# Kernel tuning notes

Measured on AMD Instinct MI355X. Metric: run time of the kernel, lower is better.

## Reference

```python
import jax, jax.numpy as jnp
import numpy as np

B, C, H, W = 1, 12, 256, 256
T = 8          # time_steps
F = 64         # recurrent/conv filters
SIGMA = 1.0


def _to_c(x):
    return jax.lax.complex(x[..., 0], x[..., 1])


def _to_r(x):
    return jnp.stack([jnp.real(x), jnp.imag(x)], axis=-1)


def _fft2c(x):  # orthogonal centered 2D FFT over last two dims (complex input)
    x = jnp.fft.ifftshift(x, axes=(-2, -1))
    x = jnp.fft.fft2(x, axes=(-2, -1), norm='ortho')
    return jnp.fft.fftshift(x, axes=(-2, -1))


def _ifft2c(x):
    x = jnp.fft.ifftshift(x, axes=(-2, -1))
    x = jnp.fft.ifft2(x, axes=(-2, -1), norm='ortho')
    return jnp.fft.fftshift(x, axes=(-2, -1))


def _conv(x, w, b=None, dilation=1):
    k = w.shape[-1]
    pad = dilation * (k - 1) // 2  # 'same' padding as ConvNonlinear
    y = jax.lax.conv_general_dilated(x, w, (1, 1), [(pad, pad), (pad, pad)],
                                     rhs_dilation=(dilation, dilation),
                                     dimension_numbers=('NCHW', 'OIHW', 'NCHW'))
    if b is not None:
        y = y + b[None, :, None, None]
    return y


def _gru(x, h, ih_w, ih_b, hh_w, hh_b):  # ConvGRUCell
    i_r, i_z, i_n = jnp.split(_conv(x, ih_w, ih_b), 3, axis=1)
    h_r, h_z, h_n = jnp.split(_conv(h, hh_w, hh_b), 3, axis=1)
    r = jax.nn.sigmoid(i_r + h_r)
    z = jax.nn.sigmoid(i_z + h_z)
    n = jnp.tanh(i_n + r * h_n)
    return (1.0 - z) * n + z * h


def setup_inputs():
    key = jax.random.key(0)
    ks = jax.random.split(key, 16)
    rn = lambda k, s, sc=1.0: jax.random.normal(k, s, jnp.float32) * sc
    return {
        'pred': rn(ks[0], (B, C, H, W, 2)),
        'masked_kspace': rn(ks[1], (B, C, H, W, 2)),
        'sense': rn(ks[2], (B, C, H, W, 2), 0.1),
        'mask': jax.random.randint(ks[3], (B, 1, H, W, 1), 0, 2).astype(bool),
        'conv1_w': rn(ks[4], (F, 4, 5, 5), 0.05),
        'conv1_b': jnp.zeros((F,), jnp.float32),
        'gru1_ih_w': rn(ks[5], (3 * F, F, 1, 1), 0.05),
        'gru1_ih_b': jnp.zeros((3 * F,), jnp.float32),
        'gru1_hh_w': rn(ks[6], (3 * F, F, 1, 1), 0.05),
        'gru1_hh_b': jnp.zeros((3 * F,), jnp.float32),
        'conv2_w': rn(ks[7], (F, F, 3, 3), 0.05),
        'conv2_b': jnp.zeros((F,), jnp.float32),
        'gru2_ih_w': rn(ks[8], (3 * F, F, 1, 1), 0.05),
        'gru2_ih_b': jnp.zeros((3 * F,), jnp.float32),
        'gru2_hh_w': rn(ks[9], (3 * F, F, 1, 1), 0.05),
        'gru2_hh_b': jnp.zeros((3 * F,), jnp.float32),
        'final_w': rn(ks[10], (2, F, 3, 3), 0.05),
        'dc_weight': jnp.ones((1,), jnp.float32),
    }


def reference(pred, masked_kspace, sense, mask, conv1_w, conv1_b, gru1_ih_w, gru1_ih_b,
              gru1_hh_w, gru1_hh_b, conv2_w, conv2_b, gru2_ih_w, gru2_ih_b, gru2_hh_w,
              gru2_hh_b, final_w, dc_weight):
    ksp_c = _to_c(masked_kspace)   # [B,C,H,W] complex
    sense_c = _to_c(sense)
    mask_f = mask[..., 0].astype(jnp.float32)  # [B,1,H,W]
    # eta init (eta=None path): coil-combined ifft of pred
    eta0 = jnp.sum(_ifft2c(_to_c(pred)) * jnp.conj(sense_c), axis=1)  # [B,H,W]
    h1_0 = jnp.zeros((B, F, H, W), jnp.float32)
    h2_0 = jnp.zeros((B, F, H, W), jnp.float32)
    inv_s2 = 1.0 / (SIGMA * SIGMA)

    def step(carry, _):
        eta, h1, h2 = carry
        # log_likelihood_gradient: SENSE-expand, fft, masked residual, ifft, coil-combine
        resid = _ifft2c(mask_f * (_fft2c(eta[:, None] * sense_c) - ksp_c))  # [B,C,H,W]
        grad = jnp.sum(resid * jnp.conj(sense_c), axis=1)                   # [B,H,W]
        g = jnp.stack([eta.real, eta.imag, grad.real, grad.imag], axis=1) * inv_s2  # [B,4,H,W]
        h1 = _gru(jax.nn.relu(_conv(g, conv1_w, conv1_b, 1)), h1,
                  gru1_ih_w, gru1_ih_b, gru1_hh_w, gru1_hh_b)
        h2 = _gru(jax.nn.relu(_conv(h1, conv2_w, conv2_b, 2)), h2,
                  gru2_ih_w, gru2_ih_b, gru2_hh_w, gru2_hh_b)
        d = _conv(h2, final_w, None, 1)  # [B,2,H,W], no bias, no nonlinearity
        eta = eta + jax.lax.complex(d[:, 0], d[:, 1])
        return (eta, h1, h2), eta

    _, etas = jax.lax.scan(step, (eta0, h1_0, h2_0), None, length=T)  # [T,B,H,W]
    # data-consistency output per time step
    soft_dc = jnp.where(mask, pred - masked_kspace, 0.0) * dc_weight[0]  # [B,C,H,W,2]
    dc_c = _to_c(soft_dc)
    out = ksp_c[None] - dc_c[None] - _fft2c(etas[:, :, None] * sense_c[None])  # [T,B,C,H,W]
    return _to_r(out)  # [T,B,C,H,W,2]
```

## Files before the change

### kernel.cpp

```cpp
#include <hip/hip_runtime.h>

#define HW 65536
#define NC 12
#define NF 64
#define NT 8
#define P2 260

typedef float2 c32;
typedef __attribute__((ext_vector_type(8))) short bf16x8;
typedef __attribute__((ext_vector_type(4))) float f32x4;

__device__ __forceinline__ float ssign(int p) {
    return ((p ^ (p >> 8)) & 1) ? -1.0f : 1.0f;
}

__device__ __forceinline__ short f2bf(float f) {
    union { float f; unsigned u; } v; v.f = f;
    unsigned r = (v.u + 0x7FFFu + ((v.u >> 16) & 1u)) >> 16;
    return (short)r;
}

__device__ __forceinline__ float bf2f(unsigned short u) {
    union { unsigned u; float f; } v; v.u = (unsigned)u << 16;
    return v.f;
}

__device__ __forceinline__ void wave_sync() {
    asm volatile("s_waitcnt lgkmcnt(0)" ::: "memory");
}

__device__ __forceinline__ void fft256_wave(c32* X, const c32* tw, int j, float conjf) {
    #pragma unroll
    for (int s = 1; s <= 8; s += 2) {
        const int H = 1 << (s - 1);
        int p = j & (H - 1);
        int r = j >> (s - 1);
        int i0 = r * 4 * H + p;
        c32 e0 = X[i0], e1 = X[i0 + H], e2 = X[i0 + 2 * H], e3 = X[i0 + 3 * H];
        c32 w = tw[p << (8 - s)];
        float wy = conjf * w.y;
        c32 t = make_float2(w.x * e1.x - wy * e1.y, w.x * e1.y + wy * e1.x);
        c32 a0 = make_float2(e0.x + t.x, e0.y + t.y);
        c32 a1 = make_float2(e0.x - t.x, e0.y - t.y);
        t = make_float2(w.x * e3.x - wy * e3.y, w.x * e3.y + wy * e3.x);
        c32 a2 = make_float2(e2.x + t.x, e2.y + t.y);
        c32 a3 = make_float2(e2.x - t.x, e2.y - t.y);
        c32 w0 = tw[p << (7 - s)];
        c32 w1 = tw[(p + H) << (7 - s)];
        float w0y = conjf * w0.y, w1y = conjf * w1.y;
        t = make_float2(w0.x * a2.x - w0y * a2.y, w0.x * a2.y + w0y * a2.x);
        X[i0]         = make_float2(a0.x + t.x, a0.y + t.y);
        X[i0 + 2 * H] = make_float2(a0.x - t.x, a0.y - t.y);
        t = make_float2(w1.x * a3.x - w1y * a3.y, w1.x * a3.y + w1y * a3.x);
        X[i0 + H]     = make_float2(a1.x + t.x, a1.y + t.y);
        X[i0 + 3 * H] = make_float2(a1.x - t.x, a1.y - t.y);
        wave_sync();
    }
}

__device__ __forceinline__ void build_tw(c32* tw, int tid) {
    if (tid < 128) {
        float a = -3.14159265358979323846f * (float)tid * (1.0f / 128.0f);
        float sv, cv;
        sincosf(a, &sv, &cv);
        tw[tid] = make_float2(cv, sv);
    }
}

__global__ __launch_bounds__(256) void fft_rows_pre(c32* __restrict__ buf,
        const c32* __restrict__ pred) {
    __shared__ c32 lds[4][256];
    __shared__ c32 tw[128];
    int tid = threadIdx.x;
    build_tw(tw, tid);
    int wid = tid >> 6, j = tid & 63;
    int r = blockIdx.x * 4 + wid;
    int coil = r >> 8, y = r & 255;
    c32* rp = buf + (size_t)r * 256;
    c32* X = lds[wid];
    #pragma unroll
    for (int e = 0; e < 4; ++e) {
        int n = (e << 6) + j;
        float s = ((n + y) & 1) ? -1.0f : 1.0f;
        c32 pv = pred[(size_t)coil * HW + y * 256 + n];
        X[__brev((unsigned)n) >> 24] = make_float2(s * pv.x, s * pv.y);
    }
    __syncthreads();
    fft256_wave(X, tw, j, -1.0f);
    #pragma unroll
    for (int e = 0; e < 4; ++e) {
        int n = (e << 6) + j;
        rp[n] = X[n];
    }
}

__global__ __launch_bounds__(256) void fft_rows_exp(c32* __restrict__ buf,
        const c32* __restrict__ eta, const c32* __restrict__ sense) {
    __shared__ c32 lds[4][256];
    __shared__ c32 tw[128];
    int tid = threadIdx.x;
    build_tw(tw, tid);
    int wid = tid >> 6, j = tid & 63;
    int r = blockIdx.x * 4 + wid;
    int coil = r >> 8, y = r & 255;
    c32* rp = buf + (size_t)r * 256;
    c32* X = lds[wid];
    #pragma unroll
    for (int e = 0; e < 4; ++e) {
        int n = (e << 6) + j;
        float s = ((n + y) & 1) ? -1.0f : 1.0f;
        c32 ev = eta[y * 256 + n];
        c32 sn = sense[(size_t)coil * HW + y * 256 + n];
        X[__brev((unsigned)n) >> 24] =
            make_float2(s * (ev.x * sn.x - ev.y * sn.y),
                        s * (ev.x * sn.y + ev.y * sn.x));
    }
    __syncthreads();
    fft256_wave(X, tw, j, 1.0f);
    #pragma unroll
    for (int e = 0; e < 4; ++e) {
        int n = (e << 6) + j;
        rp[n] = X[n];
    }
}

__global__ __launch_bounds__(256) void fft_rows_grad(const c32* __restrict__ Fk,
        const c32* __restrict__ sense, const c32* __restrict__ eta,
        short* __restrict__ gTp) {
    __shared__ c32 lds[12][256];
    __shared__ c32 tw[128];
    int tid = threadIdx.x;
    build_tw(tw, tid);
    int wid = tid >> 6, j = tid & 63;
    int y = blockIdx.x;
    #pragma unroll
    for (int cc = 0; cc < 3; ++cc) {
        int c = wid * 3 + cc;
        const c32* rp = Fk + (size_t)c * HW + y * 256;
        #pragma unroll
        for (int e = 0; e < 4; ++e) {
            int n = (e << 6) + j;
            lds[c][__brev((unsigned)n) >> 24] = rp[n];
        }
    }
    __syncthreads();
    #pragma unroll
    for (int cc = 0; cc < 3; ++cc)
        fft256_wave(&lds[wid * 3 + cc][0], tw, j, -1.0f);
    __syncthreads();
    int x = tid;
    int p = y * 256 + x;
    float ax = 0.f, ay = 0.f;
    #pragma unroll
    for (int c = 0; c < NC; ++c) {
        c32 t = lds[c][x];
        c32 s = sense[(size_t)c * HW + p];
        ax += t.x * s.x + t.y * s.y;
        ay += t.y * s.x - t.x * s.y;
    }
    float sc = (((x + y) & 1) ? -1.0f : 1.0f) * (1.0f / 256.0f);
    c32 e = eta[p];
    ushort4 o;
    o.x = (unsigned short)f2bf(e.x);
    o.y = (unsigned short)f2bf(e.y);
    o.z = (unsigned short)f2bf(ax * sc);
    o.w = (unsigned short)f2bf(ay * sc);
    ((ushort4*)gTp)[(y + 2) * P2 + x + 2] = o;
}

__global__ __launch_bounds__(256) void fft_cols(c32* __restrict__ buf, float conjf) {
    __shared__ c32 lds[8][257];
    __shared__ c32 tw[128];
    int tid = threadIdx.x;
    build_tw(tw, tid);
    c32* ip = buf + (size_t)blockIdx.y * HW;
    int x0 = blockIdx.x * 8;
    int xl = tid & 7, yb = tid >> 3;
    #pragma unroll
    for (int e = 0; e < 8; ++e) {
        int y = yb + (e << 5);
        lds[xl][__brev((unsigned)y) >> 24] = ip[y * 256 + x0 + xl];
    }
    __syncthreads();
    int wv = tid >> 6, j = tid & 63;
    #pragma unroll
    for (int cc = 0; cc < 2; ++cc)
        fft256_wave(&lds[wv * 2 + cc][0], tw, j, conjf);
    __syncthreads();
    #pragma unroll
    for (int e = 0; e < 8; ++e) {
        int y = yb + (e << 5);
        ip[y * 256 + x0 + xl] = lds[xl][y];
    }
}

__global__ __launch_bounds__(256) void fft_cols_fused(c32* __restrict__ buf,
        const c32* __restrict__ base, const c32* __restrict__ ksp,
        const int* __restrict__ mask, c32* __restrict__ outp, int write_out) {
    __shared__ c32 lds[8][257];
    __shared__ c32 tw[128];
    int tid = threadIdx.x;
    build_tw(tw, tid);
    int coil = blockIdx.y;
    c32* ip = buf + (size_t)coil * HW;
    int x0 = blockIdx.x * 8;
    int xl = tid & 7, yb = tid >> 3;
    #pragma unroll
    for (int e = 0; e < 8; ++e) {
        int y = yb + (e << 5);
        lds[xl][__brev((unsigned)y) >> 24] = ip[y * 256 + x0 + xl];
    }
    __syncthreads();
    int wv = tid >> 6, j = tid & 63;
    #pragma unroll
    for (int cc = 0; cc < 2; ++cc)
        fft256_wave(&lds[wv * 2 + cc][0], tw, j, 1.0f);
    __syncthreads();

    int x = x0 + xl;
    c32 G[8];
    #pragma unroll
    for (int e = 0; e < 8; ++e) {
        int y = yb + (e << 5);
        G[e] = lds[xl][y];
    }
    __syncthreads();
    #pragma unroll
    for (int e = 0; e < 8; ++e) {
        int y = yb + (e << 5);
        int p = y * 256 + x;
        size_t i = (size_t)coil * HW + p;
        float s = ((p ^ (p >> 8)) & 1) ? -1.0f : 1.0f;
        if (write_out) {
            c32 bv = base[i];
            float sc = s * (1.0f / 256.0f);
            outp[i] = make_float2(bv.x - sc * G[e].x, bv.y - sc * G[e].y);
        }
        c32 rv = make_float2(0.f, 0.f);
        if (mask[p]) {
            c32 k = ksp[i];
            rv = make_float2(G[e].x * (1.0f / 256.0f) - s * k.x,
                             G[e].y * (1.0f / 256.0f) - s * k.y);
        }
        lds[xl][__brev((unsigned)y) >> 24] = rv;
    }
    __syncthreads();
    #pragma unroll
    for (int cc = 0; cc < 2; ++cc)
        fft256_wave(&lds[wv * 2 + cc][0], tw, j, -1.0f);
    __syncthreads();
    #pragma unroll
    for (int e = 0; e < 8; ++e) {
        int y = yb + (e << 5);
        ip[y * 256 + x0 + xl] = lds[xl][y];
    }
}

__global__ __launch_bounds__(256) void k_combine_eta0(const c32* __restrict__ tmp,
        const c32* __restrict__ sense, c32* __restrict__ eta) {
    int p = blockIdx.x * 256 + threadIdx.x;
    float ax = 0.f, ay = 0.f;
    for (int c = 0; c < NC; ++c) {
        c32 t = tmp[c * HW + p], s = sense[c * HW + p];
        ax += t.x * s.x + t.y * s.y;
        ay += t.y * s.x - t.x * s.y;
    }
    float sc = ssign(p) * (1.0f / 256.0f);
    eta[p] = make_float2(ax * sc, ay * sc);
}

__global__ __launch_bounds__(256) void k_base(const c32* __restrict__ ksp,
        const c32* __restrict__ pred, const int* __restrict__ mask,
        const float* __restrict__ dcw, c32* __restrict__ base) {
    int i = blockIdx.x * 256 + threadIdx.x;
    int p = i & (HW - 1);
    c32 k = ksp[i];
    c32 o = k;
    if (mask[p]) {
        float w = dcw[0];
        c32 pr = pred[i];
        o.x -= (pr.x - k.x) * w;
        o.y -= (pr.y - k.y) * w;
    }
    base[i] = o;
}

__global__ __launch_bounds__(256) void k_zero_border(short* __restrict__ gTp,
        short* __restrict__ h1a, short* __restrict__ h1b,
        short* __restrict__ h2a, short* __restrict__ h2b) {
    int i = blockIdx.x * 256 + threadIdx.x;
    if (i >= 2064) return;
    int y, x;
    if (i < 1040) {
        int r = i / 260;
        y = (r < 2) ? r : 256 + r;
        x = i % 260;
    } else {
        int j = i - 1040;
        y = 2 + (j >> 2);
        int cix = j & 3;
        x = (cix < 2) ? cix : 256 + cix;
    }
    size_t px = (size_t)y * P2 + x;
    ((ushort4*)gTp)[px] = make_ushort4(0, 0, 0, 0);
    uint4 z = make_uint4(0, 0, 0, 0);
    uint4* p1 = (uint4*)(h1a + (px << 6));
    uint4* p2 = (uint4*)(h1b + (px << 6));
    uint4* p3 = (uint4*)(h2a + (px << 6));
    uint4* p4 = (uint4*)(h2b + (px << 6));
    #pragma unroll
    for (int e = 0; e < 8; ++e) { p1[e] = z; p2[e] = z; p3[e] = z; p4[e] = z; }
}

__global__ __launch_bounds__(256) void k_prep_c1(const float* __restrict__ w,
        short* __restrict__ wA) {
    int i = blockIdx.x * 256 + threadIdx.x;
    int co = i >> 7, k = i & 127;
    int tap = k >> 2, ci = k & 3;
    float v = (tap < 25) ? w[co * 100 + ci * 25 + tap] : 0.f;
    wA[i] = f2bf(v);
}

__global__ __launch_bounds__(256) void k_prep_c2(const float* __restrict__ w,
        short* __restrict__ wA) {
    int i = blockIdx.x * 256 + threadIdx.x;
    int tap = i >> 12, co = (i >> 6) & 63, ci = i & 63;
    wA[i] = f2bf(w[co * 576 + ci * 9 + tap]);
}

__global__ __launch_bounds__(256) void k_prep_cf(const float* __restrict__ w,
        short* __restrict__ wA) {
    int i = blockIdx.x * 256 + threadIdx.x;
    int tap = i >> 10, r = (i >> 6) & 15, ci = i & 63;
    float v = (r < 2) ? w[r * 576 + ci * 9 + tap] : 0.f;
    wA[i] = f2bf(v);
}

__global__ __launch_bounds__(128) void k_prep_gru(const float* __restrict__ ihw,
        const float* __restrict__ ihb, const float* __restrict__ hhw,
        const float* __restrict__ hhb, short* __restrict__ w2, float* __restrict__ bias) {
    int k = threadIdx.x;
    int r = blockIdx.x;
    int g = r >> 6, co = r & 63;
    float v = 0.f;
    if (g == 0)      v = (k < 64) ? ihw[co * 64 + k]         : hhw[co * 64 + k - 64];
    else if (g == 1) v = (k < 64) ? ihw[(64 + co) * 64 + k]  : hhw[(64 + co) * 64 + k - 64];
    else if (g == 2) v = (k < 64) ? ihw[(128 + co) * 64 + k] : 0.f;
    else             v = (k < 64) ? 0.f : hhw[(128 + co) * 64 + k - 64];
    w2[r * 128 + k] = f2bf(v);
    if (k == 0) {
        float b = (g == 0) ? ihb[co] + hhb[co]
                : (g == 1) ? ihb[64 + co] + hhb[64 + co]
                : (g == 2) ? ihb[128 + co] : hhb[128 + co];
        bias[r] = b;
    }
}

template <int NTN, bool FIRST>
__device__ __forceinline__ void gru_tail(const short (*xch)[68],
        const short* __restrict__ hprev, const short* __restrict__ w2,
        const float* __restrict__ bias, short* __restrict__ hnext,
        int wv, int lr, int lg, int px0) {
    bf16x8 A0[4], A1[4], A2[2], A3[2];
    {
        const short* w0 = w2 + (0   + wv * 16 + lr) * 128 + lg * 8;
        const short* w1 = w2 + (64  + wv * 16 + lr) * 128 + lg * 8;
        const short* w2p = w2 + (128 + wv * 16 + lr) * 128 + lg * 8;
        const short* w3 = w2 + (192 + wv * 16 + lr) * 128 + lg * 8;
        #pragma unroll
        for (int kt = 0; kt < 4; ++kt) {
            A0[kt] = *(const bf16x8*)(w0 + kt * 32);
            A1[kt] = *(const bf16x8*)(w1 + kt * 32);
        }
        A2[0] = *(const bf16x8*)(w2p);          A2[1] = *(const bf16x8*)(w2p + 32);
        A3[0] = *(const bf16x8*)(w3 + 64);      A3[1] = *(const bf16x8*)(w3 + 96);
    }

    f32x4 C0[NTN], C1[NTN], C2[NTN], C3[NTN];
    #pragma unroll
    for (int nt = 0; nt < NTN; ++nt) {
        C0[nt] = (f32x4){0.f, 0.f, 0.f, 0.f};
        C1[nt] = (f32x4){0.f, 0.f, 0.f, 0.f};
        C2[nt] = (f32x4){0.f, 0.f, 0.f, 0.f};
        C3[nt] = (f32x4){0.f, 0.f, 0.f, 0.f};
    }

    #pragma unroll
    for (int nt = 0; nt < NTN; ++nt) {
        int pxl = nt * 16 + lr;
        int px = px0 + pxl;
        int yy = px >> 8, xx = px & 255;
        size_t pb = ((size_t)((yy + 2) * P2 + (xx + 2)) << 6);
        bf16x8 B0 = *(const bf16x8*)&xch[pxl][lg * 8];
        bf16x8 B1 = *(const bf16x8*)&xch[pxl][32 + lg * 8];
        C0[nt] = __builtin_amdgcn_mfma_f32_16x16x32_bf16(A0[0], B0, C0[nt], 0, 0, 0);
        C0[nt] = __builtin_amdgcn_mfma_f32_16x16x32_bf16(A0[1], B1, C0[nt], 0, 0, 0);
        C1[nt] = __builtin_amdgcn_mfma_f32_16x16x32_bf16(A1[0], B0, C1[nt], 0, 0, 0);
        C1[nt] = __builtin_amdgcn_mfma_f32_16x16x32_bf16(A1[1], B1, C1[nt], 0, 0, 0);
        C2[nt] = __builtin_amdgcn_mfma_f32_16x16x32_bf16(A2[0], B0, C2[nt], 0, 0, 0);
        C2[nt] = __builtin_amdgcn_mfma_f32_16x16x32_bf16(A2[1], B1, C2[nt], 0, 0, 0);
        if (!FIRST) {
            bf16x8 B2 = *(const bf16x8*)(hprev + pb + lg * 8);
            bf16x8 B3 = *(const bf16x8*)(hprev + pb + 32 + lg * 8);
            C0[nt] = __builtin_amdgcn_mfma_f32_16x16x32_bf16(A0[2], B2, C0[nt], 0, 0, 0);
            C0[nt] = __builtin_amdgcn_mfma_f32_16x16x32_bf16(A0[3], B3, C0[nt], 0, 0, 0);
            C1[nt] = __builtin_amdgcn_mfma_f32_16x16x32_bf16(A1[2], B2, C1[nt], 0, 0, 0);
            C1[nt] = __builtin_amdgcn_mfma_f32_16x16x32_bf16(A1[3], B3, C1[nt], 0, 0, 0);
            C3[nt] = __builtin_amdgcn_mfma_f32_16x16x32_bf16(A3[0], B2, C3[nt], 0, 0, 0);
            C3[nt] = __builtin_amdgcn_mfma_f32_16x16x32_bf16(A3[1], B3, C3[nt], 0, 0, 0);
        }
    }

    int co = wv * 16 + lg * 4;
    float br[4], bz[4], bin_[4], bhn[4];
    #pragma unroll
    for (int i = 0; i < 4; ++i) {
        br[i]   = bias[co + i];
        bz[i]   = bias[64 + co + i];
        bin_[i] = bias[128 + co + i];
        bhn[i]  = bias[192 + co + i];
    }
    #pragma unroll
    for (int nt = 0; nt < NTN; ++nt) {
        int px = px0 + nt * 16 + lr;
        int yy = px >> 8, xx = px & 255;
        size_t pb = ((size_t)((yy + 2) * P2 + (xx + 2)) << 6);
        ushort4 hov = make_ushort4(0, 0, 0, 0);
        if (!FIRST) hov = *(const ushort4*)(hprev + pb + co);
        float ho[4] = {bf2f(hov.x), bf2f(hov.y), bf2f(hov.z), bf2f(hov.w)};
        ushort4 st;
        unsigned short* sp = &st.x;
        #pragma unroll
        for (int i = 0; i < 4; ++i) {
            float r = 1.0f / (1.0f + expf(-(C0[nt][i] + br[i])));
            float z = 1.0f / (1.0f + expf(-(C1[nt][i] + bz[i])));
            float nn = tanhf(C2[nt][i] + bin_[i] + r * (C3[nt][i] + bhn[i]));
            float hv = FIRST ? (1.0f - z) * nn : (1.0f - z) * nn + z * ho[i];
            sp[i] = (unsigned short)f2bf(hv);
        }
        *(ushort4*)(hnext + pb + co) = st;
    }
}

template <bool FIRST>
__global__ __launch_bounds__(256, 2) void conv1_gru1(const short* __restrict__ gTp,
        const short* __restrict__ wA, const float* __restrict__ cbias,
        const short* __restrict__ w2, const float* __restrict__ gbias,
        const short* __restrict__ hprev, short* __restrict__ hnext) {
    __shared__ short xch[32][68];
    int wv = threadIdx.x >> 6, l = threadIdx.x & 63;
    int lr = l & 15, lg = l >> 4;
    int y = blockIdx.x >> 3;
    int x0 = (blockIdx.x & 7) << 5;

    bf16x8 A[4];
    const short* pA = wA + (size_t)(wv * 16 + lr) * 128 + lg * 8;
    #pragma unroll
    for (int kt = 0; kt < 4; ++kt) A[kt] = *(const bf16x8*)(pA + kt * 32);

    bf16x8 B[2][4];
    #pragma unroll
    for (int nt = 0; nt < 2; ++nt) {
        int x = x0 + nt * 16 + lr;
        #pragma unroll
        for (int kt = 0; kt < 4; ++kt) {
            int t0 = kt * 8 + lg * 2;
            #pragma unroll
            for (int half = 0; half < 2; ++half) {
                int tap = t0 + half;
                int tt = (tap < 25) ? tap : 0;
                int dy = tt / 5 - 2, dx = tt % 5 - 2;
                ushort4 v = *(const ushort4*)(gTp +
                    ((size_t)((y + dy + 2) * P2 + (x + dx + 2)) << 2));
                B[nt][kt][half * 4 + 0] = (short)v.x;
                B[nt][kt][half * 4 + 1] = (short)v.y;
                B[nt][kt][half * 4 + 2] = (short)v.z;
                B[nt][kt][half * 4 + 3] = (short)v.w;
            }
        }
    }
    int co = wv * 16 + lg * 4;
    #pragma unroll
    for (int nt = 0; nt < 2; ++nt) {
        f32x4 C = (f32x4){0.f, 0.f, 0.f, 0.f};
        #pragma unroll
        for (int kt = 0; kt < 4; ++kt)
            C = __builtin_amdgcn_mfma_f32_16x16x32_bf16(A[kt], B[nt][kt], C, 0, 0, 0);
        ushort4 st;
        st.x = (unsigned short)f2bf(fmaxf(C[0] + cbias[co + 0], 0.f));
        st.y = (unsigned short)f2bf(fmaxf(C[1] + cbias[co + 1], 0.f));
        st.z = (unsigned short)f2bf(fmaxf(C[2] + cbias[co + 2], 0.f));
        st.w = (unsigned short)f2bf(fmaxf(C[3] + cbias[co + 3], 0.f));
        *(ushort4*)&xch[nt * 16 + lr][co] = st;
    }
    __syncthreads();

    gru_tail<2, FIRST>(xch, hprev, w2, gbias, hnext, wv, lr, lg, y * 256 + x0);
}

template <bool FIRST>
__global__ __launch_bounds__(256, 2) void conv2_gru2(const short* __restrict__ h1Tp,
        const short* __restrict__ wA, const float* __restrict__ cbias,
        const short* __restrict__ w2, const float* __restrict__ gbias,
        const short* __restrict__ hprev, short* __restrict__ hnext) {
    __shared__ uint4 Ld[3][68][9];
    __shared__ short xch[64][68];
    int tid = threadIdx.x;
    int wv = tid >> 6, l = tid & 63;
    int lr = l & 15, lg = l >> 4;
    int y = blockIdx.x >> 2;
    int x0 = (blockIdx.x & 3) << 6;

    for (int n = tid; n < 3 * 68 * 8; n += 256) {
        int r = n / (68 * 8);
        int rem = n - r * (68 * 8);
        int px = rem >> 3, e = rem & 7;
        const uint4* src = (const uint4*)(h1Tp +
            (((size_t)(y + 2 * r) * P2 + (x0 + px)) << 6)) + e;
        Ld[r][px][e] = *src;
    }
    __syncthreads();

    f32x4 C[4];
    #pragma unroll
    for (int nt = 0; nt < 4; ++nt) C[nt] = (f32x4){0.f, 0.f, 0.f, 0.f};

    #pragma unroll
    for (int tap = 0; tap < 9; ++tap) {
        int r = tap / 3;
        int dx = (tap % 3 - 1) * 2;
        const short* pA = wA + (size_t)(tap * 64 + wv * 16 + lr) * 64 + lg * 8;
        bf16x8 A0 = *(const bf16x8*)(pA);
        bf16x8 A1 = *(const bf16x8*)(pA + 32);
        #pragma unroll
        for (int nt = 0; nt < 4; ++nt) {
            int xl = nt * 16 + lr + dx + 2;
            bf16x8 B0 = *(const bf16x8*)&Ld[r][xl][lg];
            bf16x8 B1 = *(const bf16x8*)&Ld[r][xl][4 + lg];
            C[nt] = __builtin_amdgcn_mfma_f32_16x16x32_bf16(A0, B0, C[nt], 0, 0, 0);
            C[nt] = __builtin_amdgcn_mfma_f32_16x16x32_bf16(A1, B1, C[nt], 0, 0, 0);
        }
    }
    int co = wv * 16 + lg * 4;
    #pragma unroll
    for (int nt = 0; nt < 4; ++nt) {
        ushort4 st;
        st.x = (unsigned short)f2bf(fmaxf(C[nt][0] + cbias[co + 0], 0.f));
        st.y = (unsigned short)f2bf(fmaxf(C[nt][1] + cbias[co + 1], 0.f));
        st.z = (unsigned short)f2bf(fmaxf(C[nt][2] + cbias[co + 2], 0.f));
        st.w = (unsigned short)f2bf(fmaxf(C[nt][3] + cbias[co + 3], 0.f));
        *(ushort4*)&xch[nt * 16 + lr][co] = st;
    }
    __syncthreads();

    gru_tail<4, FIRST>(xch, hprev, w2, gbias, hnext, wv, lr, lg, y * 256 + x0);
}

__global__ __launch_bounds__(256, 2) void final_mfma(const short* __restrict__ hTp,
        const short* __restrict__ wA, c32* __restrict__ eta) {
    int wv = threadIdx.x >> 6, l = threadIdx.x & 63;
    int lr = l & 15, lg = l >> 4;
    int y = blockIdx.x >> 2;
    int x0 = (blockIdx.x & 3) << 6;
    int x = x0 + wv * 16 + lr;

    auto loadB = [&](int tap, bf16x8& b0, bf16x8& b1) {
        int dy = tap / 3 - 1, dx = tap % 3 - 1;
        const short* pB = hTp +
            ((size_t)((y + dy + 2) * P2 + (x + dx + 2)) << 6) + lg * 8;
        b0 = *(const bf16x8*)(pB);
        b1 = *(const bf16x8*)(pB + 32);
    };

    f32x4 C = (f32x4){0.f, 0.f, 0.f, 0.f};
    bf16x8 cB0, cB1;
    loadB(0, cB0, cB1);
    #pragma unroll
    for (int tap = 0; tap < 9; ++tap) {
        const short* pA = wA + (size_t)(tap * 16 + lr) * 64 + lg * 8;
        bf16x8 A0 = *(const bf16x8*)(pA);
        bf16x8 A1 = *(const bf16x8*)(pA + 32);
        bf16x8 nB0, nB1;
        if (tap < 8) loadB(tap + 1, nB0, nB1);
        C = __builtin_amdgcn_mfma_f32_16x16x32_bf16(A0, cB0, C, 0, 0, 0);
        C = __builtin_amdgcn_mfma_f32_16x16x32_bf16(A1, cB1, C, 0, 0, 0);
        if (tap < 8) { cB0 = nB0; cB1 = nB1; }
    }
    if (lg == 0) {
        int px = y * 256 + x;
        c32 e = eta[px];
        eta[px] = make_float2(e.x + C[0], e.y + C[1]);
    }
}

extern "C" void kernel_launch(void* const* d_in, const int* in_sizes, int n_in,
                              void* d_out, int out_size, void* d_ws, size_t ws_size,
                              hipStream_t stream) {
    const c32* pred   = (const c32*)d_in[0];
    const c32* ksp    = (const c32*)d_in[1];
    const c32* sense  = (const c32*)d_in[2];
    const int* mask   = (const int*)d_in[3];
    const float* c1w  = (const float*)d_in[4];
    const float* c1b  = (const float*)d_in[5];
    const float* g1iw = (const float*)d_in[6];
    const float* g1ib = (const float*)d_in[7];
    const float* g1hw = (const float*)d_in[8];
    const float* g1hb = (const float*)d_in[9];
    const float* c2w  = (const float*)d_in[10];
    const float* c2b  = (const float*)d_in[11];
    const float* g2iw = (const float*)d_in[12];
    const float* g2ib = (const float*)d_in[13];
    const float* g2hw = (const float*)d_in[14];
    const float* g2hb = (const float*)d_in[15];
    const float* fw   = (const float*)d_in[16];
    const float* dcw  = (const float*)d_in[17];

    const size_t PP = (size_t)P2 * P2;
    float* w0 = (float*)d_ws;
    c32* base = (c32*)w0;
    c32* Fk   = base + NC * HW;
    c32* tmp  = Fk + NC * HW;
    c32* eta  = tmp + NC * HW;
    short* gTp = (short*)(eta + HW);
    short* h1Ta = gTp + PP * 4;
    short* h1Tb = h1Ta + PP * 64;
    short* h2Ta = h1Tb + PP * 64;
    short* h2Tb = h2Ta + PP * 64;
    short* w2a  = h2Tb + PP * 64;
    short* w2b  = w2a + 256 * 128;
    float* biasA = (float*)(w2b + 256 * 128);
    float* biasB = biasA + 256;
    short* wAc2 = (short*)(biasB + 256);
    short* wAc1 = wAc2 + 9 * 64 * 64;
    short* wAcf = wAc1 + 64 * 128;

    dim3 B(256);
    const int gCHW = NC * HW / 256;
    const int gHW  = HW / 256;
    const int gROW = NC * 256 / 4;
    dim3 gCOL(32, NC);
    const int gC1 = HW / 32;
    const int gC2 = HW / 64;

    k_zero_border<<<9, B, 0, stream>>>(gTp, h1Ta, h1Tb, h2Ta, h2Tb);
    k_prep_gru<<<256, 128, 0, stream>>>(g1iw, g1ib, g1hw, g1hb, w2a, biasA);
    k_prep_gru<<<256, 128, 0, stream>>>(g2iw, g2ib, g2hw, g2hb, w2b, biasB);
    k_prep_c2<<<144, 256, 0, stream>>>(c2w, wAc2);
    k_prep_c1<<<32, 256, 0, stream>>>(c1w, wAc1);
    k_prep_cf<<<36, 256, 0, stream>>>(fw, wAcf);

    fft_rows_pre<<<gROW, B, 0, stream>>>(tmp, pred);
    fft_cols<<<gCOL, B, 0, stream>>>(tmp, -1.0f);
    k_combine_eta0<<<gHW, B, 0, stream>>>(tmp, sense, eta);

    k_base<<<gCHW, B, 0, stream>>>(ksp, pred, mask, dcw, base);

    fft_rows_exp<<<gROW, B, 0, stream>>>(Fk, eta, sense);
    fft_cols_fused<<<gCOL, B, 0, stream>>>(Fk, base, ksp, mask, (c32*)d_out, 0);

    short* h1c = h1Ta; short* h1n = h1Tb;
    short* h2c = h2Ta; short* h2n = h2Tb;
    c32* outp = (c32*)d_out;

    for (int t = 0; t < NT; ++t) {
        fft_rows_grad<<<gHW, B, 0, stream>>>(Fk, sense, eta, gTp);

        if (t == 0) {
            conv1_gru1<true><<<gC1, B, 0, stream>>>(gTp, wAc1, c1b, w2a, biasA, h1c, h1n);
        } else {
            conv1_gru1<false><<<gC1, B, 0, stream>>>(gTp, wAc1, c1b, w2a, biasA, h1c, h1n);
        }
        { short* s = h1c; h1c = h1n; h1n = s; }
        if (t == 0) {
            conv2_gru2<true><<<gC2, B, 0, stream>>>(h1c, wAc2, c2b, w2b, biasB, h2c, h2n);
        } else {
            conv2_gru2<false><<<gC2, B, 0, stream>>>(h1c, wAc2, c2b, w2b, biasB, h2c, h2n);
        }
        { short* s = h2c; h2c = h2n; h2n = s; }
        final_mfma<<<gC2, B, 0, stream>>>(h2c, wAcf, eta);

        fft_rows_exp<<<gROW, B, 0, stream>>>(Fk, eta, sense);
        fft_cols_fused<<<gCOL, B, 0, stream>>>(Fk, base, ksp, mask,
                                               outp + (size_t)t * NC * HW, 1);
    }
}
```

Before: 905.8 us.

## Spread each 256-point FFT across more threads in row and column kernels

```diff
diff --git a/kernel.cpp b/kernel.cpp
--- a/kernel.cpp
+++ b/kernel.cpp
@@ -58,6 +58,24 @@
     }
 }
 
+__device__ __forceinline__ void fft256_2w(c32* X, const c32* tw, int lane, float conjf) {
+    #pragma unroll
+    for (int s = 1; s <= 8; ++s) {
+        const int half = 1 << (s - 1);
+        int grp = lane >> (s - 1);
+        int pos = lane & (half - 1);
+        int i0 = (grp << s) + pos;
+        int i1 = i0 + half;
+        c32 w = tw[pos << (8 - s)];
+        float wy = conjf * w.y;
+        c32 a = X[i0], cc = X[i1];
+        c32 t = make_float2(w.x * cc.x - wy * cc.y, w.x * cc.y + wy * cc.x);
+        X[i0] = make_float2(a.x + t.x, a.y + t.y);
+        X[i1] = make_float2(a.x - t.x, a.y - t.y);
+        __syncthreads();
+    }
+}
+
 __device__ __forceinline__ void build_tw(c32* tw, int tid) {
     if (tid < 128) {
         float a = -3.14159265358979323846f * (float)tid * (1.0f / 128.0f);
@@ -69,45 +87,45 @@
 
 __global__ __launch_bounds__(256) void fft_rows_pre(c32* __restrict__ buf,
         const c32* __restrict__ pred) {
-    __shared__ c32 lds[4][256];
+    __shared__ c32 lds[2][256];
     __shared__ c32 tw[128];
     int tid = threadIdx.x;
     build_tw(tw, tid);
-    int wid = tid >> 6, j = tid & 63;
-    int r = blockIdx.x * 4 + wid;
+    int li = tid >> 7, lane = tid & 127;
+    int r = blockIdx.x * 2 + li;
     int coil = r >> 8, y = r & 255;
     c32* rp = buf + (size_t)r * 256;
-    c32* X = lds[wid];
-    #pragma unroll
-    for (int e = 0; e < 4; ++e) {
-        int n = (e << 6) + j;
+    c32* X = lds[li];
+    #pragma unroll
+    for (int e = 0; e < 2; ++e) {
+        int n = (e << 7) + lane;
         float s = ((n + y) & 1) ? -1.0f : 1.0f;
         c32 pv = pred[(size_t)coil * HW + y * 256 + n];
         X[__brev((unsigned)n) >> 24] = make_float2(s * pv.x, s * pv.y);
     }
     __syncthreads();
-    fft256_wave(X, tw, j, -1.0f);
-    #pragma unroll
-    for (int e = 0; e < 4; ++e) {
-        int n = (e << 6) + j;
+    fft256_2w(X, tw, lane, -1.0f);
+    #pragma unroll
+    for (int e = 0; e < 2; ++e) {
+        int n = (e << 7) + lane;
         rp[n] = X[n];
     }
 }
 
 __global__ __launch_bounds__(256) void fft_rows_exp(c32* __restrict__ buf,
         const c32* __restrict__ eta, const c32* __restrict__ sense) {
-    __shared__ c32 lds[4][256];
+    __shared__ c32 lds[2][256];
     __shared__ c32 tw[128];
     int tid = threadIdx.x;
     build_tw(tw, tid);
-    int wid = tid >> 6, j = tid & 63;
-    int r = blockIdx.x * 4 + wid;
+    int li = tid >> 7, lane = tid & 127;
+    int r = blockIdx.x * 2 + li;
     int coil = r >> 8, y = r & 255;
     c32* rp = buf + (size_t)r * 256;
-    c32* X = lds[wid];
-    #pragma unroll
-    for (int e = 0; e < 4; ++e) {
-        int n = (e << 6) + j;
+    c32* X = lds[li];
+    #pragma unroll
+    for (int e = 0; e < 2; ++e) {
+        int n = (e << 7) + lane;
         float s = ((n + y) & 1) ? -1.0f : 1.0f;
         c32 ev = eta[y * 256 + n];
         c32 sn = sense[(size_t)coil * HW + y * 256 + n];
@@ -116,15 +134,15 @@
                         s * (ev.x * sn.y + ev.y * sn.x));
     }
     __syncthreads();
-    fft256_wave(X, tw, j, 1.0f);
-    #pragma unroll
-    for (int e = 0; e < 4; ++e) {
-        int n = (e << 6) + j;
+    fft256_2w(X, tw, lane, 1.0f);
+    #pragma unroll
+    for (int e = 0; e < 2; ++e) {
+        int n = (e << 7) + lane;
         rp[n] = X[n];
     }
 }
 
-__global__ __launch_bounds__(256) void fft_rows_grad(const c32* __restrict__ Fk,
+__global__ __launch_bounds__(768) void fft_rows_grad(const c32* __restrict__ Fk,
         const c32* __restrict__ sense, const c32* __restrict__ eta,
         short* __restrict__ gTp) {
     __shared__ c32 lds[12][256];
@@ -133,42 +151,40 @@
     build_tw(tw, tid);
     int wid = tid >> 6, j = tid & 63;
     int y = blockIdx.x;
-    #pragma unroll
-    for (int cc = 0; cc < 3; ++cc) {
-        int c = wid * 3 + cc;
-        const c32* rp = Fk + (size_t)c * HW + y * 256;
+    {
+        const c32* rp = Fk + (size_t)wid * HW + y * 256;
         #pragma unroll
         for (int e = 0; e < 4; ++e) {
             int n = (e << 6) + j;
-            lds[c][__brev((unsigned)n) >> 24] = rp[n];
-        }
-    }
-    __syncthreads();
-    #pragma unroll
-    for (int cc = 0; cc < 3; ++cc)
-        fft256_wave(&lds[wid * 3 + cc][0], tw, j, -1.0f);
-    __syncthreads();
-    int x = tid;
-    int p = y * 256 + x;
-    float ax = 0.f, ay = 0.f;
-    #pragma unroll
-    for (int c = 0; c < NC; ++c) {
-        c32 t = lds[c][x];
-        c32 s = sense[(size_t)c * HW + p];
-        ax += t.x * s.x + t.y * s.y;
-        ay += t.y * s.x - t.x * s.y;
-    }
-    float sc = (((x + y) & 1) ? -1.0f : 1.0f) * (1.0f / 256.0f);
-    c32 e = eta[p];
-    ushort4 o;
-    o.x = (unsigned short)f2bf(e.x);
-    o.y = (unsigned short)f2bf(e.y);
-    o.z = (unsigned short)f2bf(ax * sc);
-    o.w = (unsigned short)f2bf(ay * sc);
-    ((ushort4*)gTp)[(y + 2) * P2 + x + 2] = o;
-}
-
-__global__ __launch_bounds__(256) void fft_cols(c32* __restrict__ buf, float conjf) {
+            lds[wid][__brev((unsigned)n) >> 24] = rp[n];
+        }
+    }
+    __syncthreads();
+    fft256_wave(&lds[wid][0], tw, j, -1.0f);
+    __syncthreads();
+    if (tid < 256) {
+        int x = tid;
+        int p = y * 256 + x;
+        float ax = 0.f, ay = 0.f;
+        #pragma unroll
+        for (int c = 0; c < NC; ++c) {
+            c32 t = lds[c][x];
+            c32 s = sense[(size_t)c * HW + p];
+            ax += t.x * s.x + t.y * s.y;
+            ay += t.y * s.x - t.x * s.y;
+        }
+        float sc = (((x + y) & 1) ? -1.0f : 1.0f) * (1.0f / 256.0f);
+        c32 e = eta[p];
+        ushort4 o;
+        o.x = (unsigned short)f2bf(e.x);
+        o.y = (unsigned short)f2bf(e.y);
+        o.z = (unsigned short)f2bf(ax * sc);
+        o.w = (unsigned short)f2bf(ay * sc);
+        ((ushort4*)gTp)[(y + 2) * P2 + x + 2] = o;
+    }
+}
+
+__global__ __launch_bounds__(1024) void fft_cols(c32* __restrict__ buf, float conjf) {
     __shared__ c32 lds[8][257];
     __shared__ c32 tw[128];
     int tid = threadIdx.x;
@@ -177,24 +193,21 @@
     int x0 = blockIdx.x * 8;
     int xl = tid & 7, yb = tid >> 3;
     #pragma unroll
-    for (int e = 0; e < 8; ++e) {
-        int y = yb + (e << 5);
+    for (int e = 0; e < 2; ++e) {
+        int y = yb + (e << 7);
         lds[xl][__brev((unsigned)y) >> 24] = ip[y * 256 + x0 + xl];
     }
     __syncthreads();
-    int wv = tid >> 6, j = tid & 63;
-    #pragma unroll
-    for (int cc = 0; cc < 2; ++cc)
-        fft256_wave(&lds[wv * 2 + cc][0], tw, j, conjf);
-    __syncthreads();
-    #pragma unroll
-    for (int e = 0; e < 8; ++e) {
-        int y = yb + (e << 5);
+    int col = tid >> 7, lane = tid & 127;
+    fft256_2w(&lds[col][0], tw, lane, conjf);
+    #pragma unroll
+    for (int e = 0; e < 2; ++e) {
+        int y = yb + (e << 7);
         ip[y * 256 + x0 + xl] = lds[xl][y];
     }
 }
 
-__global__ __launch_bounds__(256) void fft_cols_fused(c32* __restrict__ buf,
+__global__ __launch_bounds__(1024) void fft_cols_fused(c32* __restrict__ buf,
         const c32* __restrict__ base, const c32* __restrict__ ksp,
         const int* __restrict__ mask, c32* __restrict__ outp, int write_out) {
     __shared__ c32 lds[8][257];
@@ -206,28 +219,25 @@
     int x0 = blockIdx.x * 8;
     int xl = tid & 7, yb = tid >> 3;
     #pragma unroll
-    for (int e = 0; e < 8; ++e) {
-        int y = yb + (e << 5);
+    for (int e = 0; e < 2; ++e) {
+        int y = yb + (e << 7);
         lds[xl][__brev((unsigned)y) >> 24] = ip[y * 256 + x0 + xl];
     }
     __syncthreads();
-    int wv = tid >> 6, j = tid & 63;
-    #pragma unroll
-    for (int cc = 0; cc < 2; ++cc)
-        fft256_wave(&lds[wv * 2 + cc][0], tw, j, 1.0f);
-    __syncthreads();
+    int col = tid >> 7, lane = tid & 127;
+    fft256_2w(&lds[col][0], tw, lane, 1.0f);
 
     int x = x0 + xl;
-    c32 G[8];
-    #pragma unroll
-    for (int e = 0; e < 8; ++e) {
-        int y = yb + (e << 5);
+    c32 G[2];
+    #pragma unroll
+    for (int e = 0; e < 2; ++e) {
+        int y = yb + (e << 7);
         G[e] = lds[xl][y];
     }
     __syncthreads();
     #pragma unroll
-    for (int e = 0; e < 8; ++e) {
-        int y = yb + (e << 5);
+    for (int e = 0; e < 2; ++e) {
+        int y = yb + (e << 7);
         int p = y * 256 + x;
         size_t i = (size_t)coil * HW + p;
         float s = ((p ^ (p >> 8)) & 1) ? -1.0f : 1.0f;
@@ -245,13 +255,10 @@
         lds[xl][__brev((unsigned)y) >> 24] = rv;
     }
     __syncthreads();
-    #pragma unroll
-    for (int cc = 0; cc < 2; ++cc)
-        fft256_wave(&lds[wv * 2 + cc][0], tw, j, -1.0f);
-    __syncthreads();
-    #pragma unroll
-    for (int e = 0; e < 8; ++e) {
-        int y = yb + (e << 5);
+    fft256_2w(&lds[col][0], tw, lane, -1.0f);
+    #pragma unroll
+    for (int e = 0; e < 2; ++e) {
+        int y = yb + (e << 7);
         ip[y * 256 + x0 + xl] = lds[xl][y];
     }
 }
@@ -637,8 +644,10 @@
     dim3 B(256);
     const int gCHW = NC * HW / 256;
     const int gHW  = HW / 256;
-    const int gROW = NC * 256 / 4;
+    const int gROW = NC * 256 / 2;
     dim3 gCOL(32, NC);
+    dim3 B1024(1024);
+    dim3 B768(768);
     const int gC1 = HW / 32;
     const int gC2 = HW / 64;
 
@@ -650,20 +659,20 @@
     k_prep_cf<<<36, 256, 0, stream>>>(fw, wAcf);
 
     fft_rows_pre<<<gROW, B, 0, stream>>>(tmp, pred);
-    fft_cols<<<gCOL, B, 0, stream>>>(tmp, -1.0f);
+    fft_cols<<<gCOL, B1024, 0, stream>>>(tmp, -1.0f);
     k_combine_eta0<<<gHW, B, 0, stream>>>(tmp, sense, eta);
 
     k_base<<<gCHW, B, 0, stream>>>(ksp, pred, mask, dcw, base);
 
     fft_rows_exp<<<gROW, B, 0, stream>>>(Fk, eta, sense);
-    fft_cols_fused<<<gCOL, B, 0, stream>>>(Fk, base, ksp, mask, (c32*)d_out, 0);
+    fft_cols_fused<<<gCOL, B1024, 0, stream>>>(Fk, base, ksp, mask, (c32*)d_out, 0);
 
     short* h1c = h1Ta; short* h1n = h1Tb;
     short* h2c = h2Ta; short* h2n = h2Tb;
     c32* outp = (c32*)d_out;
 
     for (int t = 0; t < NT; ++t) {
-        fft_rows_grad<<<gHW, B, 0, stream>>>(Fk, sense, eta, gTp);
+        fft_rows_grad<<<gHW, B768, 0, stream>>>(Fk, sense, eta, gTp);
 
         if (t == 0) {
             conv1_gru1<true><<<gC1, B, 0, stream>>>(gTp, wAc1, c1b, w2a, biasA, h1c, h1n);
@@ -680,7 +689,7 @@
         final_mfma<<<gC2, B, 0, stream>>>(h2c, wAcf, eta);
 
         fft_rows_exp<<<gROW, B, 0, stream>>>(Fk, eta, sense);
-        fft_cols_fused<<<gCOL, B, 0, stream>>>(Fk, base, ksp, mask,
-                                               outp + (size_t)t * NC * HW, 1);
-    }
-}
+        fft_cols_fused<<<gCOL, B1024, 0, stream>>>(Fk, base, ksp, mask,
+                                                   outp + (size_t)t * NC * HW, 1);
+    }
+}
```

Result: faster. 884.7 us (-2.3%).
